# Performance work log

Hardware: AMD Instinct MI355X
Metric: run time of the kernel (lower is better)

## Reference

```python
import math
import jax, jax.numpy as jnp
import numpy as np

MAX_JETS = 64
BATCH = 128
HIDDEN = 128


def setup_inputs() -> dict:
    key = jax.random.key(0)
    k1, k2, k3 = jax.random.split(key, 3)
    x = jax.random.normal(k1, (MAX_JETS, BATCH, HIDDEN), dtype=jnp.float32)
    # per-event jet counts (at least 8 real jets), padding after that
    lengths = jax.random.randint(k2, (BATCH,), 8, MAX_JETS + 1)
    valid = (jnp.arange(MAX_JETS)[None, :] < lengths[:, None])  # [B, N]
    sequence_mask = valid.T[:, :, None].astype(jnp.float32)      # [N, B, 1]
    padding_mask = ~valid                                        # [B, N] True = pad
    bound = 1.0 / math.sqrt(HIDDEN)
    W = jax.random.uniform(k3, (HIDDEN, HIDDEN, HIDDEN), dtype=jnp.float32,
                           minval=-bound, maxval=bound)
    return {"x": x, "sequence_mask": sequence_mask, "W": W,
            "padding_mask": padding_mask}


def _masked_softmax(logits, mask):
    # softmax over last axis, restricted to entries where mask > 0
    neg = jnp.finfo(logits.dtype).min
    z = jnp.where(mask > 0, logits, neg)
    p = jax.nn.softmax(z, axis=-1)
    return p * mask


def _triplet_weights(xb, W):
    # symmetric_weight[i,j,k] = (sum_ab W[i,a,b] W[j,a,b]) * trace(W[k]) / d^2
    # => rank-1 in k, so the cubic einsum factorizes exactly:
    # out[b,n,m,l] = (x G x^T)[b,n,m] * (x @ t)[b,l] / (d^2 * sqrt(d))
    d = W.shape[0]
    G = jnp.einsum('nij,mij->nm', W, W)            # [d, d]
    t = jnp.trace(W, axis1=1, axis2=2)             # [d]
    P = jnp.einsum('bni,ij,bmj->bnm', xb, G, xb)   # [B, N, N]
    v = xb @ t                                     # [B, N]
    scale = 1.0 / (d * d * math.sqrt(d))
    return P[:, :, :, None] * v[:, None, None, :] * scale  # [B, N, N, N]


def reference(x, sequence_mask, W, padding_mask):
    # BranchEncoder with 0 embedding / 0 encoder layers is identity
    q = x                                           # [N, B, d]
    xb = jnp.transpose(q, (1, 0, 2))                # [B, N, d]
    weights = _triplet_weights(xb, W)               # [B, N, N, N]
    B, N = weights.shape[0], weights.shape[1]

    seq = sequence_mask[:, :, 0].T                  # [B, N]
    mask = (seq[:, None, None, :] * seq[:, None, :, None] * seq[:, :, None, None])
    idx = jnp.arange(N)
    n = idx[:, None, None]
    m = idx[None, :, None]
    l = idx[None, None, :]
    diag = (n == m) | (n == l) | (m == l)           # [N, N, N]
    mask = mask * (~diag).astype(mask.dtype)[None]

    flat = _masked_softmax(weights.reshape(B, -1), mask.reshape(B, -1))
    return flat.reshape(B, N, N, N)
```

## Files before the change

kernel.cpp:

```cpp
#include <hip/hip_runtime.h>
#include <math.h>

#define NB 128

typedef short s16x8 __attribute__((ext_vector_type(8)));
typedef float f32x16 __attribute__((ext_vector_type(16)));
typedef float f32x4 __attribute__((ext_vector_type(4)));

#define WSB_GPART 0u
#define WSB_GH    4194304u
#define WSB_T     4227072u

static __device__ __forceinline__ unsigned short f2bf(float f) {
    unsigned int u = __float_as_uint(f);
    return (unsigned short)((u + 0x7fffu + ((u >> 16) & 1u)) >> 16);
}
static __device__ __forceinline__ float bf2f(unsigned short h) {
    return __uint_as_float(((unsigned int)h) << 16);
}

__global__ __launch_bounds__(1024) void k_gram(const float* __restrict__ W,
                                               unsigned short* __restrict__ gpart,
                                               float* __restrict__ tvec) {
    __shared__ char WS[32768];
    const int blk = blockIdx.x;
    const int t = threadIdx.x;

    if (blk >= 128) {
        const int i = (blk - 128) * 64 + (t >> 4);
        const int a0 = (t & 15) * 8;
        float s = 0.f;
        #pragma unroll
        for (int a = a0; a < a0 + 8; ++a)
            s += W[(size_t)i * 16384 + a * 129];
        s += __shfl_down(s, 8, 16);
        s += __shfl_down(s, 4, 16);
        s += __shfl_down(s, 2, 16);
        s += __shfl_down(s, 1, 16);
        if ((t & 15) == 0) tvec[i] = s;
        return;
    }

    const int kc = blk;
    #pragma unroll
    for (int rep = 0; rep < 4; ++rep) {
        int ch = rep * 1024 + t;
        int row = ch >> 5, f4 = ch & 31;
        float4 w4 = *reinterpret_cast<const float4*>(
            W + (size_t)row * 16384 + kc * 128 + f4 * 4);
        ushort4 h = make_ushort4(f2bf(w4.x), f2bf(w4.y), f2bf(w4.z), f2bf(w4.w));
        *reinterpret_cast<ushort4*>(WS + row * 256 + ((f4 * 8) ^ ((row & 7) << 4))) = h;
    }
    __syncthreads();

    const int wid = t >> 6, l = t & 63;
    const int lr = l & 31, lhi = l >> 5;
    const int r = wid >> 2;
    const int c = wid & 3;

    f32x16 acc;
    #pragma unroll
    for (int i = 0; i < 16; ++i) acc[i] = 0.f;

    const int arow = r * 32 + lr;
    const int brow = c * 32 + lr;
    #pragma unroll
    for (int kk = 0; kk < 8; ++kk) {
        int kb = kk * 32 + lhi * 16;
        s16x8 a = *reinterpret_cast<const s16x8*>(WS + arow * 256 + (kb ^ ((arow & 7) << 4)));
        s16x8 bb = *reinterpret_cast<const s16x8*>(WS + brow * 256 + (kb ^ ((brow & 7) << 4)));
        acc = __builtin_amdgcn_mfma_f32_32x32x16_bf16(a, bb, acc, 0, 0, 0);
    }

    unsigned short* gp = gpart + (size_t)kc * 16384;
    #pragma unroll
    for (int reg = 0; reg < 16; ++reg) {
        int row = r * 32 + (reg & 3) + 8 * (reg >> 2) + 4 * lhi;
        gp[row * 128 + c * 32 + lr] = f2bf(acc[reg]);
    }
}

__global__ __launch_bounds__(256) void k_gred(const unsigned short* __restrict__ gpart,
                                              unsigned short* __restrict__ Gh) {
    __shared__ float red[16 * 128];
    const int blk = blockIdx.x;
    const int t = threadIdx.x;
    const int og = t & 15;
    const int cg = t >> 4;

    float acc[8];
    #pragma unroll
    for (int e = 0; e < 8; ++e) acc[e] = 0.f;

    const unsigned short* base = gpart + blk * 128 + og * 8;
    #pragma unroll
    for (int c = 0; c < 8; ++c) {
        uint4 u = *reinterpret_cast<const uint4*>(base + (size_t)(cg * 8 + c) * 16384);
        const unsigned short* hp = reinterpret_cast<const unsigned short*>(&u);
        #pragma unroll
        for (int e = 0; e < 8; ++e) acc[e] += bf2f(hp[e]);
    }
    #pragma unroll
    for (int e = 0; e < 8; ++e) red[cg * 128 + og * 8 + e] = acc[e];
    __syncthreads();

    if (t < 128) {
        float s = 0.f;
        #pragma unroll
        for (int g = 0; g < 16; ++g) s += red[g * 128 + t];
        Gh[blk * 128 + t] = f2bf(s);
    }
}

__global__ __launch_bounds__(1024) void k_pvout(const float* __restrict__ x,
                                                const unsigned short* __restrict__ Gh,
                                                const float* __restrict__ tvec,
                                                const float* __restrict__ seq,
                                                float* __restrict__ out) {
    __shared__ char XS[16384];
    __shared__ char GS[32768];
    __shared__ float PS[64 * 64];
    __shared__ float ts[128];
    __shared__ float vls[64];
    __shared__ int   flg[64];
    __shared__ float wred[16];
    __shared__ float sinv_s;
    char* YS = GS;
    const int b  = blockIdx.x;
    const int nh = blockIdx.y;
    const int t = threadIdx.x;

    #pragma unroll
    for (int rep = 0; rep < 2; ++rep) {
        int ch = rep * 1024 + t;
        int row = ch >> 5, f4 = ch & 31;
        float4 x4 = *reinterpret_cast<const float4*>(
            x + (size_t)row * 16384 + b * 128 + f4 * 4);
        ushort4 h = make_ushort4(f2bf(x4.x), f2bf(x4.y), f2bf(x4.z), f2bf(x4.w));
        *reinterpret_cast<ushort4*>(XS + row * 256 + ((f4 * 8) ^ ((row & 7) << 4))) = h;
    }
    #pragma unroll
    for (int rep = 0; rep < 2; ++rep) {
        int ch = rep * 1024 + t;
        int row = ch >> 4, kb = ch & 15;
        uint4 g4 = *reinterpret_cast<const uint4*>(Gh + row * 128 + kb * 8);
        *reinterpret_cast<uint4*>(GS + row * 256 + ((kb * 16) ^ ((row & 7) << 4))) = g4;
    }
    if (t < 128) ts[t] = tvec[t];
    __syncthreads();

    const int wid = t >> 6, l = t & 63, lr = l & 31, lhi = l >> 5;

    f32x16 acc;
    if (wid < 8) {
        #pragma unroll
        for (int i = 0; i < 16; ++i) acc[i] = 0.f;
        const int arow = (wid >> 2) * 32 + lr;
        const int brow = (wid & 3) * 32 + lr;
        #pragma unroll
        for (int kk = 0; kk < 8; ++kk) {
            int kb = kk * 32 + lhi * 16;
            s16x8 a = *reinterpret_cast<const s16x8*>(XS + arow * 256 + (kb ^ ((arow & 7) << 4)));
            s16x8 g = *reinterpret_cast<const s16x8*>(GS + brow * 256 + (kb ^ ((brow & 7) << 4)));
            acc = __builtin_amdgcn_mfma_f32_32x32x16_bf16(a, g, acc, 0, 0, 0);
        }
    } else if (wid == 8) {
        float s = 0.f;
        #pragma unroll
        for (int kb = 0; kb < 16; ++kb) {
            uint4 c4 = *reinterpret_cast<const uint4*>(
                XS + l * 256 + ((kb * 16) ^ ((l & 7) << 4)));
            const unsigned short* hp = reinterpret_cast<const unsigned short*>(&c4);
            #pragma unroll
            for (int e = 0; e < 8; ++e)
                s += bf2f(hp[e]) * ts[kb * 8 + e];
        }
        vls[l] = s;
    } else if (wid == 9) {
        flg[l] = (seq[l * NB + b] > 0.f) ? 1 : 0;
    }
    __syncthreads();

    if (wid < 8) {
        #pragma unroll
        for (int reg = 0; reg < 16; ++reg) {
            int row = (wid >> 2) * 32 + (reg & 3) + 8 * (reg >> 2) + 4 * lhi;
            int col = (wid & 3) * 32 + lr;
            *reinterpret_cast<unsigned short*>(
                YS + row * 256 + ((2 * col) ^ ((row & 7) << 4))) = f2bf(acc[reg]);
        }
    }
    __syncthreads();

    if (wid < 4) {
        f32x16 pa;
        #pragma unroll
        for (int i = 0; i < 16; ++i) pa[i] = 0.f;
        const int arow = (wid >> 1) * 32 + lr;
        const int brow = (wid & 1) * 32 + lr;
        #pragma unroll
        for (int kk = 0; kk < 8; ++kk) {
            int kb = kk * 32 + lhi * 16;
            s16x8 a = *reinterpret_cast<const s16x8*>(YS + arow * 256 + (kb ^ ((arow & 7) << 4)));
            s16x8 bb = *reinterpret_cast<const s16x8*>(XS + brow * 256 + (kb ^ ((brow & 7) << 4)));
            pa = __builtin_amdgcn_mfma_f32_32x32x16_bf16(a, bb, pa, 0, 0, 0);
        }
        const float SCALE = 1.0f / (128.0f * 128.0f * sqrtf(128.0f));
        #pragma unroll
        for (int reg = 0; reg < 16; ++reg) {
            int n = (wid >> 1) * 32 + (reg & 3) + 8 * (reg >> 2) + 4 * lhi;
            int m = (wid & 1) * 32 + lr;
            PS[n * 64 + m] = pa[reg] * SCALE;
        }
    }
    __syncthreads();

    {
        const int n = t >> 4;
        const int m0 = (t & 15) * 4;
        float a[4];
        int ok[4];
        const int fln = flg[n];
        int anyok = 0;
        #pragma unroll
        for (int j = 0; j < 4; ++j) {
            a[j] = PS[n * 64 + m0 + j];
            ok[j] = fln && flg[m0 + j] && (n != (m0 + j));
            anyok |= ok[j];
        }
        float s = 0.f;
        if (__any(anyok)) {
            for (int ll = 0; ll < 64; ++ll) {
                if (!flg[ll]) continue;
                float vv = vls[ll];
                #pragma unroll
                for (int j = 0; j < 4; ++j)
                    s += ok[j] ? __expf(a[j] * vv) : 0.f;
            }
            #pragma unroll
            for (int j = 0; j < 4; ++j)
                if (ok[j])
                    s -= __expf(a[j] * vls[n]) + __expf(a[j] * vls[m0 + j]);
        }
        #pragma unroll
        for (int off = 32; off > 0; off >>= 1) s += __shfl_down(s, off, 64);
        if (l == 0) wred[wid] = s;
        __syncthreads();
        if (t == 0) {
            float tot = 0.f;
            #pragma unroll
            for (int w = 0; w < 16; ++w) tot += wred[w];
            sinv_s = 1.0f / tot;
        }
    }
    __syncthreads();

    const float inv = sinv_s;
    const int l0 = (l & 15) * 4;
    const float vv0 = vls[l0], vv1 = vls[l0 + 1], vv2 = vls[l0 + 2], vv3 = vls[l0 + 3];
    const int   fv0 = flg[l0], fv1 = flg[l0 + 1], fv2 = flg[l0 + 2], fv3 = flg[l0 + 3];

    #pragma unroll
    for (int s = 0; s < 2; ++s) {
        const int nl = wid * 2 + s;
        const int n  = nh * 32 + nl;
        float* slabp = out + ((size_t)b << 18) + ((size_t)n << 12);
        if (!flg[n]) {
            f32x4 z = {0.f, 0.f, 0.f, 0.f};
            #pragma unroll
            for (int it = 0; it < 16; ++it)
                __builtin_nontemporal_store(z,
                    reinterpret_cast<f32x4*>(slabp + it * 256 + (l >> 4) * 64 + l0));
            continue;
        }
        #pragma unroll
        for (int it = 0; it < 16; ++it) {
            const int m = it * 4 + (l >> 4);
            const float a = PS[n * 64 + m];
            const bool okm = flg[m] && (m != n);
            f32x4 o;
            o[0] = (okm && fv0 && (l0     != n) && (l0     != m)) ? __expf(a * vv0) * inv : 0.f;
            o[1] = (okm && fv1 && (l0 + 1 != n) && (l0 + 1 != m)) ? __expf(a * vv1) * inv : 0.f;
            o[2] = (okm && fv2 && (l0 + 2 != n) && (l0 + 2 != m)) ? __expf(a * vv2) * inv : 0.f;
            o[3] = (okm && fv3 && (l0 + 3 != n) && (l0 + 3 != m)) ? __expf(a * vv3) * inv : 0.f;
            __builtin_nontemporal_store(o,
                reinterpret_cast<f32x4*>(slabp + (size_t)m * 64 + l0));
        }
    }
}

extern "C" void kernel_launch(void* const* d_in, const int* in_sizes, int n_in,
                              void* d_out, int out_size, void* d_ws, size_t ws_size,
                              hipStream_t stream) {
    const float* x   = (const float*)d_in[0];
    const float* seq = (const float*)d_in[1];
    const float* W   = (const float*)d_in[2];
    char* wsb = (char*)d_ws;
    unsigned short* gpart = (unsigned short*)(wsb + WSB_GPART);
    unsigned short* Gh    = (unsigned short*)(wsb + WSB_GH);
    float*          tvec  = (float*)(wsb + WSB_T);
    float* out = (float*)d_out;

    k_gram <<<130, 1024, 0, stream>>>(W, gpart, tvec);
    k_gred <<<128, 256, 0, stream>>>(gpart, Gh);
    k_pvout<<<dim3(128, 2), 1024, 0, stream>>>(x, Gh, tvec, seq, out);
}
```

Before: 49.40 us.

## Fuse three kernels into one cooperative kernel with grid syncs

Merges the Gram partial, Gram reduction and output kernels into a single cooperative launch of 256 blocks, using grid.sync between phases instead of separate kernel launches. Shared memory is unified into one buffer reused by each phase. The aim is to remove launch gaps and inter-kernel drain time. The cost is that grid-wide barriers can be slow, and the unified LDS of about 65KB with 1024 threads limits occupancy and must let all 256 blocks be co-resident.

```diff
diff --git a/kernel.cpp b/kernel.cpp
--- a/kernel.cpp
+++ b/kernel.cpp
@@ -1,5 +1,8 @@
 #include <hip/hip_runtime.h>
+#include <hip/hip_cooperative_groups.h>
 #include <math.h>
+
+namespace cg = cooperative_groups;
 
 #define NB 128
 
@@ -19,14 +22,63 @@
     return __uint_as_float(((unsigned int)h) << 16);
 }
 
-__global__ __launch_bounds__(1024) void k_gram(const float* __restrict__ W,
-                                               unsigned short* __restrict__ gpart,
-                                               float* __restrict__ tvec) {
-    __shared__ char WS[32768];
+__global__ __launch_bounds__(1024) void k_all(const float* __restrict__ x,
+                                              const float* __restrict__ seq,
+                                              const float* __restrict__ W,
+                                              unsigned short* __restrict__ gpart,
+                                              unsigned short* __restrict__ Gh,
+                                              float* __restrict__ tvec,
+                                              float* __restrict__ out) {
+    __shared__ __align__(16) char LDSU[66688];
+    char*  XS   = LDSU;
+    char*  GS   = LDSU + 16384;
+    float* PS   = (float*)(LDSU + 49152);
+    float* ts   = (float*)(LDSU + 65536);
+    float* vls  = (float*)(LDSU + 66048);
+    int*   flg  = (int*)  (LDSU + 66304);
+    float* wred = (float*)(LDSU + 66560);
+    float* sinv = (float*)(LDSU + 66624);
+
+    cg::grid_group grid = cg::this_grid();
     const int blk = blockIdx.x;
     const int t = threadIdx.x;
-
-    if (blk >= 128) {
+    const int wid = t >> 6, l = t & 63, lr = l & 31, lhi = l >> 5;
+
+    if (blk < 128) {
+        char* WS = GS;
+        const int kc = blk;
+        #pragma unroll
+        for (int rep = 0; rep < 4; ++rep) {
+            int ch = rep * 1024 + t;
+            int row = ch >> 5, f4 = ch & 31;
+            float4 w4 = *reinterpret_cast<const float4*>(
+                W + (size_t)row * 16384 + kc * 128 + f4 * 4);
+            ushort4 h = make_ushort4(f2bf(w4.x), f2bf(w4.y), f2bf(w4.z), f2bf(w4.w));
+            *reinterpret_cast<ushort4*>(WS + row * 256 + ((f4 * 8) ^ ((row & 7) << 4))) = h;
+        }
+        __syncthreads();
+
+        const int r = wid >> 2;
+        const int c = wid & 3;
+        f32x16 acc;
+        #pragma unroll
+        for (int i = 0; i < 16; ++i) acc[i] = 0.f;
+        const int arow = r * 32 + lr;
+        const int brow = c * 32 + lr;
+        #pragma unroll
+        for (int kk = 0; kk < 8; ++kk) {
+            int kb = kk * 32 + lhi * 16;
+            s16x8 a = *reinterpret_cast<const s16x8*>(WS + arow * 256 + (kb ^ ((arow & 7) << 4)));
+            s16x8 bb = *reinterpret_cast<const s16x8*>(WS + brow * 256 + (kb ^ ((brow & 7) << 4)));
+            acc = __builtin_amdgcn_mfma_f32_32x32x16_bf16(a, bb, acc, 0, 0, 0);
+        }
+        unsigned short* gp = gpart + (size_t)kc * 16384;
+        #pragma unroll
+        for (int reg = 0; reg < 16; ++reg) {
+            int row = r * 32 + (reg & 3) + 8 * (reg >> 2) + 4 * lhi;
+            gp[row * 128 + c * 32 + lr] = f2bf(acc[reg]);
+        }
+    } else if (blk < 130) {
         const int i = (blk - 128) * 64 + (t >> 4);
         const int a0 = (t & 15) * 8;
         float s = 0.f;
@@ -38,97 +90,50 @@
         s += __shfl_down(s, 2, 16);
         s += __shfl_down(s, 1, 16);
         if ((t & 15) == 0) tvec[i] = s;
-        return;
-    }
-
-    const int kc = blk;
-    #pragma unroll
-    for (int rep = 0; rep < 4; ++rep) {
-        int ch = rep * 1024 + t;
-        int row = ch >> 5, f4 = ch & 31;
-        float4 w4 = *reinterpret_cast<const float4*>(
-            W + (size_t)row * 16384 + kc * 128 + f4 * 4);
-        ushort4 h = make_ushort4(f2bf(w4.x), f2bf(w4.y), f2bf(w4.z), f2bf(w4.w));
-        *reinterpret_cast<ushort4*>(WS + row * 256 + ((f4 * 8) ^ ((row & 7) << 4))) = h;
-    }
-    __syncthreads();
-
-    const int wid = t >> 6, l = t & 63;
-    const int lr = l & 31, lhi = l >> 5;
-    const int r = wid >> 2;
-    const int c = wid & 3;
-
-    f32x16 acc;
-    #pragma unroll
-    for (int i = 0; i < 16; ++i) acc[i] = 0.f;
-
-    const int arow = r * 32 + lr;
-    const int brow = c * 32 + lr;
-    #pragma unroll
-    for (int kk = 0; kk < 8; ++kk) {
-        int kb = kk * 32 + lhi * 16;
-        s16x8 a = *reinterpret_cast<const s16x8*>(WS + arow * 256 + (kb ^ ((arow & 7) << 4)));
-        s16x8 bb = *reinterpret_cast<const s16x8*>(WS + brow * 256 + (kb ^ ((brow & 7) << 4)));
-        acc = __builtin_amdgcn_mfma_f32_32x32x16_bf16(a, bb, acc, 0, 0, 0);
-    }
-
-    unsigned short* gp = gpart + (size_t)kc * 16384;
-    #pragma unroll
-    for (int reg = 0; reg < 16; ++reg) {
-        int row = r * 32 + (reg & 3) + 8 * (reg >> 2) + 4 * lhi;
-        gp[row * 128 + c * 32 + lr] = f2bf(acc[reg]);
-    }
-}
-
-__global__ __launch_bounds__(256) void k_gred(const unsigned short* __restrict__ gpart,
-                                              unsigned short* __restrict__ Gh) {
-    __shared__ float red[16 * 128];
-    const int blk = blockIdx.x;
-    const int t = threadIdx.x;
-    const int og = t & 15;
-    const int cg = t >> 4;
-
-    float acc[8];
-    #pragma unroll
-    for (int e = 0; e < 8; ++e) acc[e] = 0.f;
-
-    const unsigned short* base = gpart + blk * 128 + og * 8;
-    #pragma unroll
-    for (int c = 0; c < 8; ++c) {
-        uint4 u = *reinterpret_cast<const uint4*>(base + (size_t)(cg * 8 + c) * 16384);
-        const unsigned short* hp = reinterpret_cast<const unsigned short*>(&u);
-        #pragma unroll
-        for (int e = 0; e < 8; ++e) acc[e] += bf2f(hp[e]);
-    }
-    #pragma unroll
-    for (int e = 0; e < 8; ++e) red[cg * 128 + og * 8 + e] = acc[e];
-    __syncthreads();
-
-    if (t < 128) {
-        float s = 0.f;
-        #pragma unroll
-        for (int g = 0; g < 16; ++g) s += red[g * 128 + t];
-        Gh[blk * 128 + t] = f2bf(s);
-    }
-}
-
-__global__ __launch_bounds__(1024) void k_pvout(const float* __restrict__ x,
-                                                const unsigned short* __restrict__ Gh,
-                                                const float* __restrict__ tvec,
-                                                const float* __restrict__ seq,
-                                                float* __restrict__ out) {
-    __shared__ char XS[16384];
-    __shared__ char GS[32768];
-    __shared__ float PS[64 * 64];
-    __shared__ float ts[128];
-    __shared__ float vls[64];
-    __shared__ int   flg[64];
-    __shared__ float wred[16];
-    __shared__ float sinv_s;
+    }
+
+    grid.sync();
+
+    if (blk < 128) {
+        float* red  = (float*)LDSU;
+        float* red2 = (float*)(LDSU + 32768);
+        const int og = t & 15;
+        const int cgi = t >> 4;
+        float a8[8];
+        #pragma unroll
+        for (int e = 0; e < 8; ++e) a8[e] = 0.f;
+        const unsigned short* base = gpart + blk * 128 + og * 8;
+        #pragma unroll
+        for (int c = 0; c < 2; ++c) {
+            uint4 u = *reinterpret_cast<const uint4*>(base + (size_t)(cgi * 2 + c) * 16384);
+            const unsigned short* hp = reinterpret_cast<const unsigned short*>(&u);
+            #pragma unroll
+            for (int e = 0; e < 8; ++e) a8[e] += bf2f(hp[e]);
+        }
+        #pragma unroll
+        for (int e = 0; e < 8; ++e) red[cgi * 128 + og * 8 + e] = a8[e];
+        __syncthreads();
+        {
+            const int o = t & 127, g = t >> 7;
+            float s = 0.f;
+            #pragma unroll
+            for (int j = 0; j < 8; ++j) s += red[(g * 8 + j) * 128 + o];
+            red2[g * 128 + o] = s;
+        }
+        __syncthreads();
+        if (t < 128) {
+            float s = 0.f;
+            #pragma unroll
+            for (int g = 0; g < 8; ++g) s += red2[g * 128 + t];
+            Gh[blk * 128 + t] = f2bf(s);
+        }
+    }
+
+    grid.sync();
+
+    const int b  = blk >> 1;
+    const int nh = blk & 1;
     char* YS = GS;
-    const int b  = blockIdx.x;
-    const int nh = blockIdx.y;
-    const int t = threadIdx.x;
 
     #pragma unroll
     for (int rep = 0; rep < 2; ++rep) {
@@ -148,8 +153,6 @@
     }
     if (t < 128) ts[t] = tvec[t];
     __syncthreads();
-
-    const int wid = t >> 6, l = t & 63, lr = l & 31, lhi = l >> 5;
 
     f32x16 acc;
     if (wid < 8) {
@@ -250,12 +253,12 @@
             float tot = 0.f;
             #pragma unroll
             for (int w = 0; w < 16; ++w) tot += wred[w];
-            sinv_s = 1.0f / tot;
-        }
-    }
-    __syncthreads();
-
-    const float inv = sinv_s;
+            *sinv = 1.0f / tot;
+        }
+    }
+    __syncthreads();
+
+    const float inv = *sinv;
     const int l0 = (l & 15) * 4;
     const float vv0 = vls[l0], vv1 = vls[l0 + 1], vv2 = vls[l0 + 2], vv3 = vls[l0 + 3];
     const int   fv0 = flg[l0], fv1 = flg[l0 + 1], fv2 = flg[l0 + 2], fv3 = flg[l0 + 3];
@@ -301,7 +304,8 @@
     float*          tvec  = (float*)(wsb + WSB_T);
     float* out = (float*)d_out;
 
-    k_gram <<<130, 1024, 0, stream>>>(W, gpart, tvec);
-    k_gred <<<128, 256, 0, stream>>>(gpart, Gh);
-    k_pvout<<<dim3(128, 2), 1024, 0, stream>>>(x, Gh, tvec, seq, out);
+    void* args[] = {(void*)&x, (void*)&seq, (void*)&W, (void*)&gpart,
+                    (void*)&Gh, (void*)&tvec, (void*)&out};
+    hipLaunchCooperativeKernel((const void*)k_all, dim3(256), dim3(1024),
+                               args, 0, stream);
 }
```

New measurement: 118.7 us. +140.2%, slower.

## Fuse Gram partial and reduction kernels via grid-wide atomic barrier

Applied to the files above, without the earlier changes.

Merges the per-chunk Gram MFMA kernel and the cross-chunk reduction kernel into one launch. A global atomic counter acts as a grid barrier so every block waits until all 128 partials are written, then reduces its own row using all 1024 threads with a two-stage LDS reduction. This removes one kernel launch and its drain gap, but adds a memset of the counter and relies on all 130 blocks being co-resident, which risks deadlock if they are not.

```diff
diff --git a/kernel.cpp b/kernel.cpp
--- a/kernel.cpp
+++ b/kernel.cpp
@@ -10,6 +10,7 @@
 #define WSB_GPART 0u
 #define WSB_GH    4194304u
 #define WSB_T     4227072u
+#define WSB_CNT   4227584u
 
 static __device__ __forceinline__ unsigned short f2bf(float f) {
     unsigned int u = __float_as_uint(f);
@@ -19,10 +20,12 @@
     return __uint_as_float(((unsigned int)h) << 16);
 }
 
-__global__ __launch_bounds__(1024) void k_gram(const float* __restrict__ W,
-                                               unsigned short* __restrict__ gpart,
-                                               float* __restrict__ tvec) {
-    __shared__ char WS[32768];
+__global__ __launch_bounds__(1024) void k_gramred(const float* __restrict__ W,
+                                                  unsigned short* __restrict__ gpart,
+                                                  unsigned short* __restrict__ Gh,
+                                                  float* __restrict__ tvec,
+                                                  unsigned int* __restrict__ cnt) {
+    __shared__ __align__(16) char LDSB[36864];
     const int blk = blockIdx.x;
     const int t = threadIdx.x;
 
@@ -41,6 +44,7 @@
         return;
     }
 
+    char* WS = LDSB;
     const int kc = blk;
     #pragma unroll
     for (int rep = 0; rep < 4; ++rep) {
@@ -53,62 +57,72 @@
     }
     __syncthreads();
 
-    const int wid = t >> 6, l = t & 63;
-    const int lr = l & 31, lhi = l >> 5;
-    const int r = wid >> 2;
-    const int c = wid & 3;
-
-    f32x16 acc;
-    #pragma unroll
-    for (int i = 0; i < 16; ++i) acc[i] = 0.f;
-
-    const int arow = r * 32 + lr;
-    const int brow = c * 32 + lr;
-    #pragma unroll
-    for (int kk = 0; kk < 8; ++kk) {
-        int kb = kk * 32 + lhi * 16;
-        s16x8 a = *reinterpret_cast<const s16x8*>(WS + arow * 256 + (kb ^ ((arow & 7) << 4)));
-        s16x8 bb = *reinterpret_cast<const s16x8*>(WS + brow * 256 + (kb ^ ((brow & 7) << 4)));
-        acc = __builtin_amdgcn_mfma_f32_32x32x16_bf16(a, bb, acc, 0, 0, 0);
-    }
-
-    unsigned short* gp = gpart + (size_t)kc * 16384;
-    #pragma unroll
-    for (int reg = 0; reg < 16; ++reg) {
-        int row = r * 32 + (reg & 3) + 8 * (reg >> 2) + 4 * lhi;
-        gp[row * 128 + c * 32 + lr] = f2bf(acc[reg]);
-    }
-}
-
-__global__ __launch_bounds__(256) void k_gred(const unsigned short* __restrict__ gpart,
-                                              unsigned short* __restrict__ Gh) {
-    __shared__ float red[16 * 128];
-    const int blk = blockIdx.x;
-    const int t = threadIdx.x;
-    const int og = t & 15;
-    const int cg = t >> 4;
-
-    float acc[8];
-    #pragma unroll
-    for (int e = 0; e < 8; ++e) acc[e] = 0.f;
-
-    const unsigned short* base = gpart + blk * 128 + og * 8;
-    #pragma unroll
-    for (int c = 0; c < 8; ++c) {
-        uint4 u = *reinterpret_cast<const uint4*>(base + (size_t)(cg * 8 + c) * 16384);
-        const unsigned short* hp = reinterpret_cast<const unsigned short*>(&u);
-        #pragma unroll
-        for (int e = 0; e < 8; ++e) acc[e] += bf2f(hp[e]);
-    }
-    #pragma unroll
-    for (int e = 0; e < 8; ++e) red[cg * 128 + og * 8 + e] = acc[e];
-    __syncthreads();
-
-    if (t < 128) {
-        float s = 0.f;
-        #pragma unroll
-        for (int g = 0; g < 16; ++g) s += red[g * 128 + t];
-        Gh[blk * 128 + t] = f2bf(s);
+    {
+        const int wid = t >> 6, l = t & 63;
+        const int lr = l & 31, lhi = l >> 5;
+        const int r = wid >> 2;
+        const int c = wid & 3;
+        f32x16 acc;
+        #pragma unroll
+        for (int i = 0; i < 16; ++i) acc[i] = 0.f;
+        const int arow = r * 32 + lr;
+        const int brow = c * 32 + lr;
+        #pragma unroll
+        for (int kk = 0; kk < 8; ++kk) {
+            int kb = kk * 32 + lhi * 16;
+            s16x8 a = *reinterpret_cast<const s16x8*>(WS + arow * 256 + (kb ^ ((arow & 7) << 4)));
+            s16x8 bb = *reinterpret_cast<const s16x8*>(WS + brow * 256 + (kb ^ ((brow & 7) << 4)));
+            acc = __builtin_amdgcn_mfma_f32_32x32x16_bf16(a, bb, acc, 0, 0, 0);
+        }
+        unsigned short* gp = gpart + (size_t)kc * 16384;
+        #pragma unroll
+        for (int reg = 0; reg < 16; ++reg) {
+            int row = r * 32 + (reg & 3) + 8 * (reg >> 2) + 4 * lhi;
+            gp[row * 128 + c * 32 + lr] = f2bf(acc[reg]);
+        }
+    }
+    __syncthreads();
+
+    if (t == 0) {
+        __hip_atomic_fetch_add(cnt, 1u, __ATOMIC_RELEASE, __HIP_MEMORY_SCOPE_AGENT);
+        while (__hip_atomic_load(cnt, __ATOMIC_ACQUIRE, __HIP_MEMORY_SCOPE_AGENT) < 128u)
+            __builtin_amdgcn_s_sleep(32);
+    }
+    __syncthreads();
+
+    {
+        float* red  = (float*)LDSB;
+        float* red2 = (float*)(LDSB + 32768);
+        const int og  = t & 15;
+        const int cgi = t >> 4;
+        float a8[8];
+        #pragma unroll
+        for (int e = 0; e < 8; ++e) a8[e] = 0.f;
+        const unsigned short* base = gpart + blk * 128 + og * 8;
+        #pragma unroll
+        for (int c = 0; c < 2; ++c) {
+            uint4 u = *reinterpret_cast<const uint4*>(base + (size_t)(cgi * 2 + c) * 16384);
+            const unsigned short* hp = reinterpret_cast<const unsigned short*>(&u);
+            #pragma unroll
+            for (int e = 0; e < 8; ++e) a8[e] += bf2f(hp[e]);
+        }
+        #pragma unroll
+        for (int e = 0; e < 8; ++e) red[cgi * 128 + og * 8 + e] = a8[e];
+        __syncthreads();
+        {
+            const int o = t & 127, g = t >> 7;
+            float s = 0.f;
+            #pragma unroll
+            for (int j = 0; j < 8; ++j) s += red[(g * 8 + j) * 128 + o];
+            red2[g * 128 + o] = s;
+        }
+        __syncthreads();
+        if (t < 128) {
+            float s = 0.f;
+            #pragma unroll
+            for (int g = 0; g < 8; ++g) s += red2[g * 128 + t];
+            Gh[blk * 128 + t] = f2bf(s);
+        }
     }
 }
 
@@ -299,9 +313,10 @@
     unsigned short* gpart = (unsigned short*)(wsb + WSB_GPART);
     unsigned short* Gh    = (unsigned short*)(wsb + WSB_GH);
     float*          tvec  = (float*)(wsb + WSB_T);
+    unsigned int*   cnt   = (unsigned int*)(wsb + WSB_CNT);
     float* out = (float*)d_out;
 
-    k_gram <<<130, 1024, 0, stream>>>(W, gpart, tvec);
-    k_gred <<<128, 256, 0, stream>>>(gpart, Gh);
-    k_pvout<<<dim3(128, 2), 1024, 0, stream>>>(x, Gh, tvec, seq, out);
-}
+    hipMemsetAsync((void*)cnt, 0, 4, stream);
+    k_gramred<<<130, 1024, 0, stream>>>(W, gpart, Gh, tvec, cnt);
+    k_pvout  <<<dim3(128, 2), 1024, 0, stream>>>(x, Gh, tvec, seq, out);
+}
```

New measurement: 58.34 us. +18.1%, slower.
